# Kernel tuning notes

Measured on AMD Instinct MI355X. Metric: run time of the kernel, lower is better.

## Reference

```python
import jax, jax.numpy as jnp
import numpy as np

N_NODES = 16384
DIM = 1024
NUM_HEADS = 16
HEAD_DIM = 64
CURV = -1.0  # hyperbolic stereographic (Poincare ball) curvature, shared by all heads
EPS = 1e-15
PROJ_EPS = 4e-3  # geoopt float32 projection eps


def _clamp_abs(x, eps):
    # geoopt.utils.clamp_abs: sign-preserving clamp of |x| (sign(0) -> +1)
    s = jnp.sign(jnp.sign(x) + 0.5)
    return s * jnp.maximum(jnp.abs(x), eps)


def _artan_k(x, k):  # k < 0: artanh(sqrt(-k) x)/sqrt(-k)
    sk = jnp.sqrt(jnp.maximum(jnp.abs(k), EPS))
    return jnp.arctanh(jnp.clip(sk * x, -1.0 + 1e-7, 1.0 - 1e-7)) / sk


def _tan_k(x, k):  # k < 0: tanh(sqrt(-k) x)/sqrt(-k)
    sk = jnp.sqrt(jnp.maximum(jnp.abs(k), EPS))
    return jnp.tanh(sk * x) / sk


def _norm(x):
    return jnp.maximum(jnp.linalg.norm(x, axis=-1, keepdims=True), EPS)


def _project(x, k):
    maxnorm = (1.0 - PROJ_EPS) / jnp.sqrt(jnp.maximum(jnp.abs(k), EPS))
    n = _norm(x)
    return jnp.where(n > maxnorm, x / n * maxnorm, x)


def _mobius_scalar_mul(r, x, k):
    xn = _norm(x)
    return _tan_k(r * _artan_k(xn, k), k) * x / xn


def _mobius_matvec(W, x, k):
    xn = _norm(x)
    mx = x @ W
    mxn = _norm(mx)
    res = _tan_k(mxn / xn * _artan_k(xn, k), k) * mx / mxn
    zero = jnp.all(mx == 0, axis=-1, keepdims=True)
    return jnp.where(zero, jnp.zeros((), x.dtype), res)


def _logmap0(y, k):
    yn = _norm(y)
    return _artan_k(yn, k) * y / yn


def _expmap0(u, k):
    un = _norm(u)
    return _project(_tan_k(un, k) * u / un, k)


def _kappa_relu(x, k):
    # manifold.apply(relu): relu in tangent space at origin
    return _expmap0(jax.nn.relu(_logmap0(x, k)), k)


def _geo_lin_attn(Q, K, V, mask, k):
    # Q,K,V: (H,N,hd); mask: (N,); k: (H,1,1)
    denom_pt = jnp.maximum(1.0 + k * jnp.sum(V * V, -1, keepdims=True), EPS)  # (H,N,1)
    v1 = jax.nn.elu(Q / denom_pt) + 1.0          # parallel_transport0back(V, Q) -> elu+1
    gamma = 2.0 / denom_pt                        # lambda_x(V)
    denominator = _clamp_abs(gamma - 1.0, 1e-10)
    m = mask[None, :, None]
    x = gamma / denominator * V * m
    v2 = denominator * (jax.nn.elu(K / denom_pt) + 1.0) * m
    v2_sum = jnp.sum(v2, axis=-2)                 # (H,hd)
    D = jnp.einsum('hnd,hd->hn', v1, v2_sum)
    D_inv = 1.0 / jnp.where(D == 0, 1e-5, D)
    context = jnp.einsum('hnd,hne->hde', v2, x)   # (H,hd,hd)
    out = jnp.einsum('hde,hnd,hn->hne', context, v1, D_inv)
    out = _project(out, k)
    out = _mobius_scalar_mul(0.5, out, k)
    return _project(out, k)


def setup_inputs():
    key = jax.random.key(0)
    ks = jax.random.split(key, 6)
    kc = jnp.float32(CURV)
    X = _project(0.02 * jax.random.normal(ks[0], (N_NODES, DIM), jnp.float32), kc)
    mask = jnp.ones((N_NODES,), jnp.float32)
    hdim = NUM_HEADS * HEAD_DIM
    Wq = 0.02 * jax.random.normal(ks[1], (DIM, hdim), jnp.float32)
    bq = jnp.zeros((hdim,), jnp.float32)
    Wk = 0.02 * jax.random.normal(ks[2], (DIM, hdim), jnp.float32)
    bk = jnp.zeros((hdim,), jnp.float32)
    Wv = 0.01 * jax.random.normal(ks[3], (DIM, hdim), jnp.float32)
    Wff = 0.01 * jax.random.normal(ks[4], (hdim, DIM), jnp.float32)
    return {"X": X, "mask": mask, "Wq": Wq, "bq": bq, "Wk": Wk, "bk": bk, "Wv": Wv, "Wff": Wff}


def reference(X, mask, Wq, bq, Wk, bk, Wv, Wff):
    kc = jnp.float32(CURV)
    k_head = jnp.full((NUM_HEADS, 1, 1), CURV, X.dtype)

    def split(t):  # (N, H*hd) -> (H, N, hd)
        return t.reshape(N_NODES, NUM_HEADS, HEAD_DIM).transpose(1, 0, 2)

    Q = split(X @ Wq + bq)
    K = split(X @ Wk + bk)
    V = split(_kappa_relu(_mobius_matvec(Wv, X, kc), kc))  # KappaGCN with A_hat=None
    attn = _geo_lin_attn(Q, K, V, mask, k_head)            # (H,N,hd)
    comb = attn.transpose(1, 0, 2).reshape(N_NODES, NUM_HEADS * HEAD_DIM)
    return _kappa_relu(_mobius_matvec(Wff, comb, kc), kc)
```

## Files before the change

kernel.cpp:

```cpp
#include <hip/hip_runtime.h>
#include <hip/hip_bf16.h>
#include <math.h>

#define N_NODES 16384
#define DIMV 1024
#define NHEADS 16
#define HEADD 64

typedef __attribute__((ext_vector_type(8))) short short8;
typedef __attribute__((ext_vector_type(4))) float f32x4;
typedef unsigned short ushort_t;

#define GLD16(gptr, lptr)                                                                 \
  __builtin_amdgcn_global_load_lds((const __attribute__((address_space(1))) void*)(gptr), \
                                   (__attribute__((address_space(3))) void*)(lptr), 16, 0, 0)


__device__ __forceinline__ float waveReduceSum(float v) {
#pragma unroll
  for (int m = 32; m; m >>= 1) v += __shfl_xor(v, m);
  return v;
}

__device__ __forceinline__ float blockReduceSum(float v, float* red) {
  float w = waveReduceSum(v);
  __syncthreads();
  if ((threadIdx.x & 63) == 0) red[threadIdx.x >> 6] = w;
  __syncthreads();
  return red[0] + red[1] + red[2] + red[3];
}

__device__ __forceinline__ float elup1_fast(float z) {
  return z > 0.0f ? z + 1.0f : __expf(z);
}

__device__ __forceinline__ float clampabs(float x, float eps) {
  float s = (x >= 0.0f) ? 1.0f : -1.0f;
  return s * fmaxf(fabsf(x), eps);
}

__device__ __forceinline__ ushort_t f2b(float x) {
  unsigned u = __float_as_uint(x);
  unsigned r = (u + 0x7FFFu + ((u >> 16) & 1u)) >> 16;
  return (ushort_t)r;
}
__device__ __forceinline__ float b2f(ushort_t h) {
  return __uint_as_float(((unsigned)h) << 16);
}

__global__ __launch_bounds__(256) void cvt_norm_kernel(const float* __restrict__ src,
                                                       ushort_t* __restrict__ dst,
                                                       float* __restrict__ rowsq) {
  __shared__ float red[4];
  const int row = blockIdx.x;
  const int t = threadIdx.x;
  float4 x4 = ((const float4*)(src + (size_t)row * DIMV))[t];
  ushort_t h[4] = {f2b(x4.x), f2b(x4.y), f2b(x4.z), f2b(x4.w)};
  ((uint2*)(dst + (size_t)row * DIMV))[t] = *(uint2*)h;
  float s = x4.x * x4.x + x4.y * x4.y + x4.z * x4.z + x4.w * x4.w;
  s = blockReduceSum(s, red);
  if (t == 0) rowsq[row] = s;
}

__global__ __launch_bounds__(256) void transW_kernel(const float* __restrict__ src,
                                                     ushort_t* __restrict__ hi) {
  __shared__ float tile[32][33];
  const int bx = blockIdx.x * 32, by = blockIdx.y * 32;
  const int tx = threadIdx.x & 31, ty = threadIdx.x >> 5;
#pragma unroll
  for (int i = 0; i < 32; i += 8) tile[ty + i][tx] = src[(size_t)(by + ty + i) * DIMV + bx + tx];
  __syncthreads();
#pragma unroll
  for (int i = 0; i < 32; i += 8)
    hi[(size_t)(bx + ty + i) * DIMV + by + tx] = f2b(tile[tx][ty + i]);
}

__global__ __launch_bounds__(256) void transW3_kernel(const float* __restrict__ s0,
                                                      const float* __restrict__ s1,
                                                      const float* __restrict__ s2,
                                                      ushort_t* __restrict__ d0,
                                                      ushort_t* __restrict__ d1,
                                                      ushort_t* __restrict__ d2) {
  __shared__ float tile[32][33];
  const float* src = (blockIdx.z == 0) ? s0 : (blockIdx.z == 1) ? s1 : s2;
  ushort_t* dst = (blockIdx.z == 0) ? d0 : (blockIdx.z == 1) ? d1 : d2;
  const int bx = blockIdx.x * 32, by = blockIdx.y * 32;
  const int tx = threadIdx.x & 31, ty = threadIdx.x >> 5;
#pragma unroll
  for (int i = 0; i < 32; i += 8) tile[ty + i][tx] = src[(size_t)(by + ty + i) * DIMV + bx + tx];
  __syncthreads();
#pragma unroll
  for (int i = 0; i < 32; i += 8)
    dst[(size_t)(bx + ty + i) * DIMV + by + tx] = f2b(tile[tx][ty + i]);
}


template <int EPI, int NB>
__global__ __launch_bounds__(512, 2) void gemm_bf(const ushort_t* __restrict__ A,
                                                  const ushort_t* __restrict__ Bt,
                                                  const float* __restrict__ biasQ,
                                                  const float* __restrict__ biasK,
                                                  const float* __restrict__ denom,
                                                  const float* __restrict__ mask,
                                                  float* __restrict__ v2sum,
                                                  float* __restrict__ mxhsq,
                                                  float* __restrict__ reluhsq,
                                                  ushort_t* __restrict__ Cq,
                                                  ushort_t* __restrict__ Ck) {
  __shared__ ushort_t As[2][256 * 64];
  __shared__ ushort_t Bs[2][256 * 64];
  const int bid = blockIdx.x;
  const int nwg = NB * 64;
  const int swz = (bid & 7) * (nwg / 8) + (bid >> 3);
  const int bm = (swz / NB) * 256;
  const int bn = (swz % NB) * 256;
  const int t = threadIdx.x;
  const int w = t >> 6, lane = t & 63, l15 = lane & 15;
  const int wr = (w >> 2) * 128;
  const int wcn = (w & 3) * 64;
  const int g4 = lane >> 4;
  const int e7 = l15 & 7;
  const int uo0 = (g4 ^ e7) * 8;
  const int uo1 = ((4 + g4) ^ e7) * 8;

  const int rowin = lane >> 3;
  const int ksh = ((lane & 7) ^ ((lane >> 3) & 7)) * 8;
  const ushort_t *gA[4], *gB[4];
  int lofs[4];
#pragma unroll
  for (int c = 0; c < 4; ++c) {
    const int ch = w + 8 * c;
    lofs[c] = ch * 512;
    gA[c] = A + (size_t)(bm + ch * 8 + rowin) * DIMV + ksh;
    gB[c] = Bt + (size_t)(bn + ch * 8 + rowin) * DIMV + ksh;
  }

#define STAGE_G(buf, k0)                              \
  do {                                                \
    _Pragma("unroll") for (int c = 0; c < 4; ++c) {   \
      GLD16(gA[c] + (k0), &As[buf][lofs[c]]);         \
      GLD16(gB[c] + (k0), &Bs[buf][lofs[c]]);         \
    }                                                 \
  } while (0)

  f32x4 acc[8][4];
#pragma unroll
  for (int i = 0; i < 8; ++i)
#pragma unroll
    for (int j = 0; j < 4; ++j) acc[i][j] = (f32x4){0.f, 0.f, 0.f, 0.f};

  STAGE_G(0, 0);
  __syncthreads();
  int cur = 0;
  for (int k0 = 0; k0 < DIMV; k0 += 64) {
    if (k0 + 64 < DIMV) STAGE_G(cur ^ 1, k0 + 64);
#pragma unroll
    for (int ks = 0; ks < 2; ++ks) {
      const int uo = ks ? uo1 : uo0;
      short8 bf[4];
#pragma unroll
      for (int j = 0; j < 4; ++j)
        bf[j] = *(const short8*)&Bs[cur][(wcn + j * 16 + l15) * 64 + uo];
#pragma unroll
      for (int i = 0; i < 8; ++i) {
        short8 af = *(const short8*)&As[cur][(wr + i * 16 + l15) * 64 + uo];
#pragma unroll
        for (int j = 0; j < 4; ++j)
          acc[i][j] = __builtin_amdgcn_mfma_f32_16x16x32_bf16(af, bf[j], acc[i][j], 0, 0, 0);
      }
    }
    __syncthreads();
    cur ^= 1;
  }
#undef STAGE_G

  const int rbase = (lane >> 4) * 4;
  if (EPI == 0) {
#pragma unroll
    for (int j = 0; j < 4; ++j) {
      const int col = bn + wcn + j * 16 + l15;
#pragma unroll
      for (int i = 0; i < 8; ++i)
#pragma unroll
        for (int r = 0; r < 4; ++r)
          Cq[(size_t)(bm + wr + i * 16 + rbase + r) * DIMV + col] = f2b(acc[i][j][r]);
    }
  } else if (EPI == 4) {
    const int h = ((bn + wcn) >> 6) & (NHEADS - 1);
#pragma unroll
    for (int i = 0; i < 8; ++i) {
#pragma unroll
      for (int r = 0; r < 4; ++r) {
        const int row = bm + wr + i * 16 + rbase + r;
        float smx = 0.f, srel = 0.f;
#pragma unroll
        for (int j = 0; j < 4; ++j) {
          float val = acc[i][j][r];
          Cq[(size_t)row * DIMV + bn + wcn + j * 16 + l15] = f2b(val);
          smx = fmaf(val, val, smx);
          float rv = fmaxf(val, 0.f);
          srel = fmaf(rv, rv, srel);
        }
        smx += __shfl_xor(smx, 1); smx += __shfl_xor(smx, 2);
        smx += __shfl_xor(smx, 4); smx += __shfl_xor(smx, 8);
        srel += __shfl_xor(srel, 1); srel += __shfl_xor(srel, 2);
        srel += __shfl_xor(srel, 4); srel += __shfl_xor(srel, 8);
        if (l15 == 0) {
          mxhsq[(size_t)h * N_NODES + row] = smx;
          reluhsq[(size_t)h * N_NODES + row] = srel;
        }
      }
    }
  } else {
    const bool isK = (bn >= DIMV);
    const int h = ((bn + wcn) >> 6) & (NHEADS - 1);
    int lc[4];
    float bb[4];
#pragma unroll
    for (int j = 0; j < 4; ++j) {
      lc[j] = (bn + wcn + j * 16 + l15) & (DIMV - 1);
      bb[j] = isK ? biasK[lc[j]] : biasQ[lc[j]];
    }
    float csum[4] = {0.f, 0.f, 0.f, 0.f};
#pragma unroll
    for (int i = 0; i < 8; ++i) {
#pragma unroll
      for (int r = 0; r < 4; ++r) {
        const int row = bm + wr + i * 16 + rbase + r;
        const float invdp = 1.0f / denom[(size_t)h * N_NODES + row];
        float den = 0.f, mk = 0.f;
        if (isK) {
          den = clampabs(2.0f * invdp - 1.0f, 1e-10f);
          mk = mask[row];
        }
#pragma unroll
        for (int j = 0; j < 4; ++j) {
          float val = elup1_fast((acc[i][j][r] + bb[j]) * invdp);
          if (isK) {
            val = den * val * mk;
            csum[j] += val;
            Ck[(size_t)row * DIMV + lc[j]] = f2b(val);
          } else {
            Cq[(size_t)row * DIMV + lc[j]] = f2b(val);
          }
        }
      }
    }
    if (isK) {
#pragma unroll
      for (int j = 0; j < 4; ++j) atomicAdd(&v2sum[lc[j]], csum[j]);
    }
  }
}

__global__ __launch_bounds__(256) void vscale_kernel(const float* __restrict__ xnormsq,
                                                     const float* __restrict__ mxhsq,
                                                     const float* __restrict__ reluhsq,
                                                     float* __restrict__ scaleV,
                                                     float* __restrict__ denom) {
  const int row = blockIdx.x * 256 + threadIdx.x;
  float sm = 0.f, sr = 0.f;
  float hs[NHEADS];
#pragma unroll
  for (int h = 0; h < NHEADS; ++h) {
    sm += mxhsq[(size_t)h * N_NODES + row];
    hs[h] = reluhsq[(size_t)h * N_NODES + row];
    sr += hs[h];
  }
  float sx = xnormsq[row];
  float xn = fmaxf(sqrtf(sx), 1e-15f);
  float mxn = fmaxf(sqrtf(sm), 1e-15f);
  float cx = fminf(xn, 1.0f - 1e-7f);
  float t1 = tanhf(mxn / xn * atanhf(cx));
  float s1 = t1 / mxn;
  float yn = fmaxf(fabsf(t1), 1e-15f);
  float a = atanhf(fminf(yn, 1.0f - 1e-7f)) / yn;
  float k1 = a * s1;
  float un = fmaxf(k1 * sqrtf(sr), 1e-15f);
  float t2 = tanhf(un);
  float s2 = t2 / un;
  if (t2 > 0.996f) s2 *= 0.996f / t2;
  float sV = s2 * k1;
  scaleV[row] = sV;
#pragma unroll
  for (int h = 0; h < NHEADS; ++h)
    denom[(size_t)h * N_NODES + row] = fmaxf(1.0f - sV * sV * hs[h], 1e-15f);
}

__global__ __launch_bounds__(256) void rowtrans_kernel(const ushort_t* __restrict__ msrc,
                                                       const float* __restrict__ rowsq,
                                                       float* __restrict__ dstv) {
  __shared__ float red[4];
  const int row = blockIdx.x;
  const int t = threadIdx.x;
  uint2 mraw = ((const uint2*)(msrc + (size_t)row * DIMV))[t];
  ushort_t* mh = (ushort_t*)&mraw;
  float4 m4 = make_float4(b2f(mh[0]), b2f(mh[1]), b2f(mh[2]), b2f(mh[3]));
  float sm = m4.x * m4.x + m4.y * m4.y + m4.z * m4.z + m4.w * m4.w;
  sm = blockReduceSum(sm, red);
  float sx = rowsq[row];

  float xn = fmaxf(sqrtf(sx), 1e-15f);
  float mxn = fmaxf(sqrtf(sm), 1e-15f);
  float cx = fminf(xn, 1.0f - 1e-7f);
  float t1 = tanhf(mxn / xn * atanhf(cx));
  float s1 = t1 / mxn;

  float yn = fmaxf(fabsf(t1), 1e-15f);
  float a = atanhf(fminf(yn, 1.0f - 1e-7f)) / yn;
  float k1 = a * s1;
  float4 u = make_float4(fmaxf(k1 * m4.x, 0.0f), fmaxf(k1 * m4.y, 0.0f),
                         fmaxf(k1 * m4.z, 0.0f), fmaxf(k1 * m4.w, 0.0f));
  float su = u.x * u.x + u.y * u.y + u.z * u.z + u.w * u.w;
  su = blockReduceSum(su, red);

  float un = fmaxf(sqrtf(su), 1e-15f);
  float t2 = tanhf(un);
  float s2 = t2 / un;
  if (t2 > 0.996f) s2 *= 0.996f / t2;
  float4 o = make_float4(s2 * u.x, s2 * u.y, s2 * u.z, s2 * u.w);
  ((float4*)(dstv + (size_t)row * DIMV))[t] = o;
}

__global__ __launch_bounds__(256) void context_kernel(const ushort_t* __restrict__ v2buf,
                                                      const ushort_t* __restrict__ mxVbuf,
                                                      const float* __restrict__ scaleV,
                                                      const float* __restrict__ denom,
                                                      const float* __restrict__ mask,
                                                      float* __restrict__ ctxT) {
  __shared__ ushort_t s2T[64 * 64];
  __shared__ ushort_t sxT[64 * 64];
  const int h = blockIdx.y;
  const int t = threadIdx.x;
  const int w = t >> 6, lane = t & 63, l15 = lane & 15, g = lane >> 4;
  const int e7 = l15 & 7;
  const int uo0 = (g ^ e7) * 8;
  const int uo1 = ((4 + g) ^ e7) * 8;

  f32x4 acc[4];
#pragma unroll
  for (int j = 0; j < 4; ++j) acc[j] = (f32x4){0.f, 0.f, 0.f, 0.f};

  const int rbase = blockIdx.x * 512;
  for (int c = 0; c < 8; ++c) {
#pragma unroll
    for (int i = 0; i < 4; ++i) {
      int f = i * 256 + t;
      int r = f >> 4;
      int cc = (f & 15) * 4;
      int row = rbase + c * 64 + r;
      uint2 araw = *(const uint2*)(v2buf + (size_t)row * DIMV + h * HEADD + cc);
      ushort_t* ah = (ushort_t*)&araw;
      float dp = denom[(size_t)h * N_NODES + row];
      float gamma = 2.0f / dp;
      float den = clampabs(gamma - 1.0f, 1e-10f);
      float c1 = gamma / den * mask[row] * scaleV[row];
      uint2 braw = *(const uint2*)(mxVbuf + (size_t)row * DIMV + h * HEADD + cc);
      ushort_t* bh = (ushort_t*)&braw;
      const int rhi = r >> 3, rlo = r & 7;
#pragma unroll
      for (int q = 0; q < 4; ++q) {
        const int d = cc + q;
        const int pos = d * 64 + ((rhi ^ (d & 7)) << 3) + rlo;
        s2T[pos] = ah[q];
        sxT[pos] = f2b(c1 * fmaxf(b2f(bh[q]), 0.f));
      }
    }
    __syncthreads();
#pragma unroll
    for (int ks = 0; ks < 2; ++ks) {
      const int uo = ks ? uo1 : uo0;
      short8 af = *(const short8*)&s2T[(w * 16 + l15) * 64 + uo];
#pragma unroll
      for (int j = 0; j < 4; ++j) {
        short8 bfv = *(const short8*)&sxT[(j * 16 + l15) * 64 + uo];
        acc[j] = __builtin_amdgcn_mfma_f32_16x16x32_bf16(af, bfv, acc[j], 0, 0, 0);
      }
    }
    __syncthreads();
  }
#pragma unroll
  for (int j = 0; j < 4; ++j)
#pragma unroll
    for (int r = 0; r < 4; ++r)
      atomicAdd(&ctxT[h * 4096 + (j * 16 + l15) * 64 + w * 16 + g * 4 + r], acc[j][r]);
}

__global__ __launch_bounds__(256) void out_mfma_kernel(const ushort_t* __restrict__ v1bf,
                                                       const float* __restrict__ v2sum,
                                                       const float* __restrict__ ctxT,
                                                       ushort_t* __restrict__ combHi,
                                                       float* __restrict__ combnorm) {
  __shared__ ushort_t Blds[80][88];
  const int h = blockIdx.y;
  const int bm = blockIdx.x * 256;
  const int t = threadIdx.x;
  const int w = t >> 6, lane = t & 63, l15 = lane & 15;
  const int kk = (lane >> 4) * 8;

  for (int idx = t; idx < 80 * 64; idx += 256) {
    int e = idx >> 6, d = idx & 63;
    float v = 0.0f;
    if (e < 64) v = ctxT[h * 4096 + e * 64 + d];
    else if (e == 64) v = v2sum[h * 64 + d];
    Blds[e][d] = f2b(v);
  }
  __syncthreads();

  f32x4 acc[4][5];
#pragma unroll
  for (int i = 0; i < 4; ++i)
#pragma unroll
    for (int j = 0; j < 5; ++j) acc[i][j] = (f32x4){0.f, 0.f, 0.f, 0.f};
#pragma unroll
  for (int ks = 0; ks < 2; ++ks) {
    short8 bfr[5];
#pragma unroll
    for (int j = 0; j < 5; ++j) bfr[j] = *(const short8*)&Blds[j * 16 + l15][ks * 32 + kk];
#pragma unroll
    for (int i = 0; i < 4; ++i) {
      short8 af = *(const short8*)(v1bf + (size_t)(bm + w * 64 + i * 16 + l15) * DIMV +
                                   h * HEADD + ks * 32 + kk);
#pragma unroll
      for (int j = 0; j < 5; ++j)
        acc[i][j] = __builtin_amdgcn_mfma_f32_16x16x32_bf16(af, bfr[j], acc[i][j], 0, 0, 0);
    }
  }

  const int g4 = (lane >> 4) * 4;
#pragma unroll
  for (int i = 0; i < 4; ++i) {
#pragma unroll
    for (int r = 0; r < 4; ++r) {
      const int row = bm + w * 64 + i * 16 + g4 + r;
      float D = __shfl(acc[i][4][r], lane & 48);
      float Dinv = 1.0f / (D == 0.0f ? 1e-5f : D);
      float o[4];
      float s = 0.0f;
#pragma unroll
      for (int j = 0; j < 4; ++j) {
        o[j] = acc[i][j][r] * Dinv;
        s = fmaf(o[j], o[j], s);
      }
      s += __shfl_xor(s, 1); s += __shfl_xor(s, 2);
      s += __shfl_xor(s, 4); s += __shfl_xor(s, 8);
      float n1 = fmaxf(sqrtf(s), 1e-15f);
      float sc = 1.0f;
      if (n1 > 0.996f) sc = 0.996f / n1;
      float xn = fmaxf(fminf(n1, 0.996f), 1e-15f);
      float cx = fminf(xn, 1.0f - 1e-7f);
      float t2 = cx / (1.0f + sqrtf(1.0f - cx * cx));
      sc *= t2 / xn;
      if (l15 == 0) atomicAdd(&combnorm[row], s * sc * sc);
#pragma unroll
      for (int j = 0; j < 4; ++j) {
        float ov = o[j] * sc;
        combHi[(size_t)row * DIMV + h * HEADD + j * 16 + l15] = f2b(ov);
      }
    }
  }
}


extern "C" void kernel_launch(void* const* d_in, const int* in_sizes, int n_in,
                              void* d_out, int out_size, void* d_ws, size_t ws_size,
                              hipStream_t stream) {
  const float* X = (const float*)d_in[0];
  const float* mask = (const float*)d_in[1];
  const float* Wq = (const float*)d_in[2];
  const float* bq = (const float*)d_in[3];
  const float* Wk = (const float*)d_in[4];
  const float* bk = (const float*)d_in[5];
  const float* Wv = (const float*)d_in[6];
  const float* Wff = (const float*)d_in[7];
  float* out = (float*)d_out;

  const size_t MAT = (size_t)N_NODES * DIMV;
  char* p = (char*)d_ws;
  ushort_t* v1bf = (ushort_t*)p;
  ushort_t* mxV = (ushort_t*)(p + MAT * 2);
  float* combnorm = (float*)(p + MAT * 2);
  p += MAT * 4;
  float* xnormsq = (float*)p;
  ushort_t* v2bf = (ushort_t*)p;
  ushort_t* combHi = (ushort_t*)p;
  p += MAT * 4;
  ushort_t* WffHi = (ushort_t*)p;
  p += MAT * 2;
  ushort_t* Xbf = (ushort_t*)p;
  ushort_t* outBf = Xbf;
  p += MAT * 2;
  float* denom = (float*)p;   p += (size_t)NHEADS * N_NODES * 4;
  float* v2sum = (float*)p;   p += 1024 * 4;
  float* ctxT = (float*)p;    p += (size_t)NHEADS * 4096 * 4;
  float* mxhsq = (float*)p;   p += (size_t)NHEADS * N_NODES * 4;
  float* reluhsq = (float*)p; p += (size_t)NHEADS * N_NODES * 4;
  float* scaleV = (float*)p;  p += (size_t)N_NODES * 4;
  const size_t need = (size_t)(p - (char*)d_ws);
  if (ws_size < need) return;

  ushort_t* Wt = (ushort_t*)d_out;
  ushort_t* WtK = Wt + (size_t)DIMV * DIMV;
  ushort_t* WtV = WtK + (size_t)DIMV * DIMV;

  dim3 tgrid(32, 32);

  cvt_norm_kernel<<<N_NODES, 256, 0, stream>>>(X, Xbf, xnormsq);
  transW3_kernel<<<dim3(32, 32, 3), 256, 0, stream>>>(Wq, Wk, Wv, Wt, WtK, WtV);
  gemm_bf<4, 4><<<256, 512, 0, stream>>>(Xbf, WtV, nullptr, nullptr, nullptr, nullptr,
                                         nullptr, mxhsq, reluhsq, mxV, nullptr);
  vscale_kernel<<<N_NODES / 256, 256, 0, stream>>>(xnormsq, mxhsq, reluhsq, scaleV, denom);
  hipMemsetAsync(v2sum, 0, (1024 + 4096 * NHEADS) * sizeof(float), stream);
  gemm_bf<3, 8><<<512, 512, 0, stream>>>(Xbf, Wt, bq, bk, denom, mask, v2sum, nullptr,
                                         nullptr, v1bf, v2bf);
  context_kernel<<<dim3(32, NHEADS), 256, 0, stream>>>(v2bf, mxV, scaleV, denom, mask, ctxT);
  hipMemsetAsync(combnorm, 0, N_NODES * sizeof(float), stream);
  out_mfma_kernel<<<dim3(N_NODES / 256, NHEADS), 256, 0, stream>>>(v1bf, v2sum, ctxT, combHi,
                                                                   combnorm);
  transW_kernel<<<tgrid, 256, 0, stream>>>(Wff, WffHi);
  gemm_bf<0, 4><<<256, 512, 0, stream>>>(combHi, WffHi, nullptr, nullptr, nullptr, nullptr,
                                         nullptr, nullptr, nullptr, outBf, nullptr);
  rowtrans_kernel<<<N_NODES, 256, 0, stream>>>(outBf, combnorm, out);
}
```

Before: 350.2 us.

## Compute Q/K projection GEMM in FP8 e4m3 with swizzled layout

Converts X and the transposed Wq/Wk to scaled FP8 e4m3 in a pre-swizzled LDS-friendly layout, and runs the fused Q/K projection GEMM with fp8 MFMA instructions, descaling by 1/256 in the epilogue. It also folds the Wff transpose into the same multi-weight transpose launch, removing one kernel launch. The aim is to halve operand bytes and double MFMA throughput for the largest GEMM, at the cost of reduced precision in Q and K. The scratch layout changes (Xf8 placed in the output buffer), which risks accuracy tolerance failures.

```diff
diff --git a/kernel.cpp b/kernel.cpp
--- a/kernel.cpp
+++ b/kernel.cpp
@@ -9,7 +9,9 @@
 
 typedef __attribute__((ext_vector_type(8))) short short8;
 typedef __attribute__((ext_vector_type(4))) float f32x4;
+typedef __attribute__((ext_vector_type(2))) long long2_t;
 typedef unsigned short ushort_t;
+typedef unsigned char uchar_t;
 
 #define GLD16(gptr, lptr)                                                                 \
   __builtin_amdgcn_global_load_lds((const __attribute__((address_space(1))) void*)(gptr), \
@@ -48,8 +50,22 @@
   return __uint_as_float(((unsigned)h) << 16);
 }
 
+__device__ __forceinline__ uchar_t f2e4m3(float x) {
+  unsigned u = __float_as_uint(x);
+  unsigned s = (u >> 24) & 0x80u;
+  unsigned a = u & 0x7fffffffu;
+  if (a < 0x3c800000u) return (uchar_t)s;
+  if (a > 0x43e00000u) return (uchar_t)(s | 0x7eu);
+  unsigned lsb = (a >> 20) & 1u;
+  a += 0x7ffffu + lsb;
+  unsigned e = (a >> 23) - 120u;
+  unsigned m = (a >> 20) & 7u;
+  return (uchar_t)(s | (e << 3) | m);
+}
+
 __global__ __launch_bounds__(256) void cvt_norm_kernel(const float* __restrict__ src,
                                                        ushort_t* __restrict__ dst,
+                                                       uchar_t* __restrict__ xf8,
                                                        float* __restrict__ rowsq) {
   __shared__ float red[4];
   const int row = blockIdx.x;
@@ -57,56 +73,57 @@
   float4 x4 = ((const float4*)(src + (size_t)row * DIMV))[t];
   ushort_t h[4] = {f2b(x4.x), f2b(x4.y), f2b(x4.z), f2b(x4.w)};
   ((uint2*)(dst + (size_t)row * DIMV))[t] = *(uint2*)h;
+  unsigned pk = (unsigned)f2e4m3(x4.x * 16.f) | ((unsigned)f2e4m3(x4.y * 16.f) << 8) |
+                ((unsigned)f2e4m3(x4.z * 16.f) << 16) | ((unsigned)f2e4m3(x4.w * 16.f) << 24);
+  const int g = (t >> 1) & 3, ks = (t >> 3) & 1, k64 = t >> 4, e0 = (t & 1) << 2;
+  *(unsigned*)(xf8 + (size_t)row * DIMV + k64 * 64 + ((g ^ ((row >> 1) & 3)) << 4) +
+               (ks << 3) + e0) = pk;
   float s = x4.x * x4.x + x4.y * x4.y + x4.z * x4.z + x4.w * x4.w;
   s = blockReduceSum(s, red);
   if (t == 0) rowsq[row] = s;
 }
 
-__global__ __launch_bounds__(256) void transW_kernel(const float* __restrict__ src,
-                                                     ushort_t* __restrict__ hi) {
+__global__ __launch_bounds__(256) void transW4_kernel(const float* __restrict__ s0,
+                                                      const float* __restrict__ s1,
+                                                      const float* __restrict__ s2,
+                                                      const float* __restrict__ s3,
+                                                      uchar_t* __restrict__ d0,
+                                                      uchar_t* __restrict__ d1,
+                                                      ushort_t* __restrict__ d2,
+                                                      ushort_t* __restrict__ d3) {
   __shared__ float tile[32][33];
+  const int z = blockIdx.z;
+  const float* src = (z == 0) ? s0 : (z == 1) ? s1 : (z == 2) ? s2 : s3;
   const int bx = blockIdx.x * 32, by = blockIdx.y * 32;
   const int tx = threadIdx.x & 31, ty = threadIdx.x >> 5;
 #pragma unroll
   for (int i = 0; i < 32; i += 8) tile[ty + i][tx] = src[(size_t)(by + ty + i) * DIMV + bx + tx];
   __syncthreads();
-#pragma unroll
-  for (int i = 0; i < 32; i += 8)
-    hi[(size_t)(bx + ty + i) * DIMV + by + tx] = f2b(tile[tx][ty + i]);
-}
-
-__global__ __launch_bounds__(256) void transW3_kernel(const float* __restrict__ s0,
-                                                      const float* __restrict__ s1,
-                                                      const float* __restrict__ s2,
-                                                      ushort_t* __restrict__ d0,
-                                                      ushort_t* __restrict__ d1,
-                                                      ushort_t* __restrict__ d2) {
-  __shared__ float tile[32][33];
-  const float* src = (blockIdx.z == 0) ? s0 : (blockIdx.z == 1) ? s1 : s2;
-  ushort_t* dst = (blockIdx.z == 0) ? d0 : (blockIdx.z == 1) ? d1 : d2;
-  const int bx = blockIdx.x * 32, by = blockIdx.y * 32;
-  const int tx = threadIdx.x & 31, ty = threadIdx.x >> 5;
-#pragma unroll
-  for (int i = 0; i < 32; i += 8) tile[ty + i][tx] = src[(size_t)(by + ty + i) * DIMV + bx + tx];
-  __syncthreads();
-#pragma unroll
-  for (int i = 0; i < 32; i += 8)
-    dst[(size_t)(bx + ty + i) * DIMV + by + tx] = f2b(tile[tx][ty + i]);
+  if (z < 2) {
+    uchar_t* dst = z ? d1 : d0;
+#pragma unroll
+    for (int i = 0; i < 32; i += 8) {
+      const int n = bx + ty + i, k = by + tx;
+      const size_t byte = (size_t)n * DIMV + ((k >> 6) << 6) +
+                          ((((k >> 3) & 3) ^ ((n >> 1) & 3)) << 4) + (((k >> 5) & 1) << 3) +
+                          (k & 7);
+      dst[byte] = f2e4m3(16.f * tile[tx][ty + i]);
+    }
+  } else {
+    ushort_t* dst = (z == 2) ? d2 : d3;
+#pragma unroll
+    for (int i = 0; i < 32; i += 8)
+      dst[(size_t)(bx + ty + i) * DIMV + by + tx] = f2b(tile[tx][ty + i]);
+  }
 }
 
 
 template <int EPI, int NB>
 __global__ __launch_bounds__(512, 2) void gemm_bf(const ushort_t* __restrict__ A,
                                                   const ushort_t* __restrict__ Bt,
-                                                  const float* __restrict__ biasQ,
-                                                  const float* __restrict__ biasK,
-                                                  const float* __restrict__ denom,
-                                                  const float* __restrict__ mask,
-                                                  float* __restrict__ v2sum,
                                                   float* __restrict__ mxhsq,
                                                   float* __restrict__ reluhsq,
-                                                  ushort_t* __restrict__ Cq,
-                                                  ushort_t* __restrict__ Ck) {
+                                                  ushort_t* __restrict__ Cq) {
   __shared__ ushort_t As[2][256 * 64];
   __shared__ ushort_t Bs[2][256 * 64];
   const int bid = blockIdx.x;
@@ -185,7 +202,7 @@
         for (int r = 0; r < 4; ++r)
           Cq[(size_t)(bm + wr + i * 16 + rbase + r) * DIMV + col] = f2b(acc[i][j][r]);
     }
-  } else if (EPI == 4) {
+  } else {
     const int h = ((bn + wcn) >> 6) & (NHEADS - 1);
 #pragma unroll
     for (int i = 0; i < 8; ++i) {
@@ -211,45 +228,117 @@
         }
       }
     }
-  } else {
-    const bool isK = (bn >= DIMV);
-    const int h = ((bn + wcn) >> 6) & (NHEADS - 1);
-    int lc[4];
-    float bb[4];
-#pragma unroll
-    for (int j = 0; j < 4; ++j) {
-      lc[j] = (bn + wcn + j * 16 + l15) & (DIMV - 1);
-      bb[j] = isK ? biasK[lc[j]] : biasQ[lc[j]];
-    }
-    float csum[4] = {0.f, 0.f, 0.f, 0.f};
+  }
+}
+
+template <int NB>
+__global__ __launch_bounds__(512, 2) void gemm_f8qk(const uchar_t* __restrict__ Xf8,
+                                                    const uchar_t* __restrict__ Bt8,
+                                                    const float* __restrict__ biasQ,
+                                                    const float* __restrict__ biasK,
+                                                    const float* __restrict__ denom,
+                                                    const float* __restrict__ mask,
+                                                    float* __restrict__ v2sum,
+                                                    ushort_t* __restrict__ Cq,
+                                                    ushort_t* __restrict__ Ck) {
+  __shared__ uchar_t LB[65536];
+  const int bid = blockIdx.x;
+  const int nwg = NB * 64;
+  const int swz = (bid & 7) * (nwg / 8) + (bid >> 3);
+  const int bm = (swz / NB) * 256;
+  const int bn = (swz % NB) * 256;
+  const int t = threadIdx.x;
+  const int w = t >> 6, lane = t & 63, l15 = lane & 15;
+  const int wr = (w >> 2) * 128;
+  const int wcn = (w & 3) * 64;
+  const int g = lane >> 4;
+  const int aoff = ((g ^ ((l15 >> 1) & 3)) << 4);
+
+  const uchar_t *gA[2], *gB[2];
+  int lofs[2];
+#pragma unroll
+  for (int c = 0; c < 2; ++c) {
+    const int row = (t >> 2) + c * 128;
+    lofs[c] = t * 16 + c * 8192;
+    gA[c] = Xf8 + (size_t)(bm + row) * DIMV + (t & 3) * 16;
+    gB[c] = Bt8 + (size_t)(bn + row) * DIMV + (t & 3) * 16;
+  }
+
+#define STAGE_F(buf, kb)                                        \
+  do {                                                          \
+    _Pragma("unroll") for (int c = 0; c < 2; ++c) {             \
+      GLD16(gA[c] + (kb), &LB[(buf) * 16384 + lofs[c]]);        \
+      GLD16(gB[c] + (kb), &LB[32768 + (buf) * 16384 + lofs[c]]); \
+    }                                                           \
+  } while (0)
+
+  f32x4 acc[8][4];
+#pragma unroll
+  for (int i = 0; i < 8; ++i)
+#pragma unroll
+    for (int j = 0; j < 4; ++j) acc[i][j] = (f32x4){0.f, 0.f, 0.f, 0.f};
+
+  STAGE_F(0, 0);
+  __syncthreads();
+  int cur = 0;
+  for (int kt = 0; kt < 16; ++kt) {
+    if (kt < 15) STAGE_F(cur ^ 1, (kt + 1) * 64);
+    long2_t bf[4];
+#pragma unroll
+    for (int j = 0; j < 4; ++j)
+      bf[j] = *(const long2_t*)&LB[32768 + cur * 16384 + (wcn + j * 16 + l15) * 64 + aoff];
 #pragma unroll
     for (int i = 0; i < 8; ++i) {
-#pragma unroll
-      for (int r = 0; r < 4; ++r) {
-        const int row = bm + wr + i * 16 + rbase + r;
-        const float invdp = 1.0f / denom[(size_t)h * N_NODES + row];
-        float den = 0.f, mk = 0.f;
+      long2_t af = *(const long2_t*)&LB[cur * 16384 + (wr + i * 16 + l15) * 64 + aoff];
+#pragma unroll
+      for (int j = 0; j < 4; ++j) {
+        acc[i][j] = __builtin_amdgcn_mfma_f32_16x16x32_fp8_fp8(af.x, bf[j].x, acc[i][j], 0, 0, 0);
+        acc[i][j] = __builtin_amdgcn_mfma_f32_16x16x32_fp8_fp8(af.y, bf[j].y, acc[i][j], 0, 0, 0);
+      }
+    }
+    __syncthreads();
+    cur ^= 1;
+  }
+#undef STAGE_F
+
+  const int rbase = (lane >> 4) * 4;
+  const bool isK = (bn >= DIMV);
+  const int h = ((bn + wcn) >> 6) & (NHEADS - 1);
+  int lc[4];
+  float bb[4];
+#pragma unroll
+  for (int j = 0; j < 4; ++j) {
+    lc[j] = (bn + wcn + j * 16 + l15) & (DIMV - 1);
+    bb[j] = isK ? biasK[lc[j]] : biasQ[lc[j]];
+  }
+  float csum[4] = {0.f, 0.f, 0.f, 0.f};
+#pragma unroll
+  for (int i = 0; i < 8; ++i) {
+#pragma unroll
+    for (int r = 0; r < 4; ++r) {
+      const int row = bm + wr + i * 16 + rbase + r;
+      const float invdp = 1.0f / denom[(size_t)h * N_NODES + row];
+      float den = 0.f, mk = 0.f;
+      if (isK) {
+        den = clampabs(2.0f * invdp - 1.0f, 1e-10f);
+        mk = mask[row];
+      }
+#pragma unroll
+      for (int j = 0; j < 4; ++j) {
+        float val = elup1_fast((acc[i][j][r] * 0.00390625f + bb[j]) * invdp);
         if (isK) {
-          den = clampabs(2.0f * invdp - 1.0f, 1e-10f);
-          mk = mask[row];
+          val = den * val * mk;
+          csum[j] += val;
+          Ck[(size_t)row * DIMV + lc[j]] = f2b(val);
+        } else {
+          Cq[(size_t)row * DIMV + lc[j]] = f2b(val);
         }
-#pragma unroll
-        for (int j = 0; j < 4; ++j) {
-          float val = elup1_fast((acc[i][j][r] + bb[j]) * invdp);
-          if (isK) {
-            val = den * val * mk;
-            csum[j] += val;
-            Ck[(size_t)row * DIMV + lc[j]] = f2b(val);
-          } else {
-            Cq[(size_t)row * DIMV + lc[j]] = f2b(val);
-          }
-        }
-      }
-    }
-    if (isK) {
-#pragma unroll
-      for (int j = 0; j < 4; ++j) atomicAdd(&v2sum[lc[j]], csum[j]);
-    }
+      }
+    }
+  }
+  if (isK) {
+#pragma unroll
+    for (int j = 0; j < 4; ++j) atomicAdd(&v2sum[lc[j]], csum[j]);
   }
 }
 
@@ -483,9 +572,8 @@
   p += MAT * 4;
   float* xnormsq = (float*)p;
   ushort_t* v2bf = (ushort_t*)p;
+  p += MAT * 4;
   ushort_t* combHi = (ushort_t*)p;
-  p += MAT * 4;
-  ushort_t* WffHi = (ushort_t*)p;
   p += MAT * 2;
   ushort_t* Xbf = (ushort_t*)p;
   ushort_t* outBf = Xbf;
@@ -499,26 +587,22 @@
   const size_t need = (size_t)(p - (char*)d_ws);
   if (ws_size < need) return;
 
-  ushort_t* Wt = (ushort_t*)d_out;
-  ushort_t* WtK = Wt + (size_t)DIMV * DIMV;
-  ushort_t* WtV = WtK + (size_t)DIMV * DIMV;
-
-  dim3 tgrid(32, 32);
-
-  cvt_norm_kernel<<<N_NODES, 256, 0, stream>>>(X, Xbf, xnormsq);
-  transW3_kernel<<<dim3(32, 32, 3), 256, 0, stream>>>(Wq, Wk, Wv, Wt, WtK, WtV);
-  gemm_bf<4, 4><<<256, 512, 0, stream>>>(Xbf, WtV, nullptr, nullptr, nullptr, nullptr,
-                                         nullptr, mxhsq, reluhsq, mxV, nullptr);
+  uchar_t* Wq8 = (uchar_t*)d_out;
+  uchar_t* Wk8 = Wq8 + (size_t)DIMV * DIMV;
+  ushort_t* WtV = (ushort_t*)(Wq8 + 2 * (size_t)DIMV * DIMV);
+  ushort_t* WffT = WtV + (size_t)DIMV * DIMV;
+  uchar_t* Xf8 = (uchar_t*)d_out + 8 * 1024 * 1024;
+
+  cvt_norm_kernel<<<N_NODES, 256, 0, stream>>>(X, Xbf, Xf8, xnormsq);
+  transW4_kernel<<<dim3(32, 32, 4), 256, 0, stream>>>(Wq, Wk, Wv, Wff, Wq8, Wk8, WtV, WffT);
+  gemm_bf<4, 4><<<256, 512, 0, stream>>>(Xbf, WtV, mxhsq, reluhsq, mxV);
   vscale_kernel<<<N_NODES / 256, 256, 0, stream>>>(xnormsq, mxhsq, reluhsq, scaleV, denom);
   hipMemsetAsync(v2sum, 0, (1024 + 4096 * NHEADS) * sizeof(float), stream);
-  gemm_bf<3, 8><<<512, 512, 0, stream>>>(Xbf, Wt, bq, bk, denom, mask, v2sum, nullptr,
-                                         nullptr, v1bf, v2bf);
+  gemm_f8qk<8><<<512, 512, 0, stream>>>(Xf8, Wq8, bq, bk, denom, mask, v2sum, v1bf, v2bf);
   context_kernel<<<dim3(32, NHEADS), 256, 0, stream>>>(v2bf, mxV, scaleV, denom, mask, ctxT);
   hipMemsetAsync(combnorm, 0, N_NODES * sizeof(float), stream);
   out_mfma_kernel<<<dim3(N_NODES / 256, NHEADS), 256, 0, stream>>>(v1bf, v2sum, ctxT, combHi,
                                                                    combnorm);
-  transW_kernel<<<tgrid, 256, 0, stream>>>(Wff, WffHi);
-  gemm_bf<0, 4><<<256, 512, 0, stream>>>(combHi, WffHi, nullptr, nullptr, nullptr, nullptr,
-                                         nullptr, nullptr, nullptr, outBf, nullptr);
+  gemm_bf<0, 4><<<256, 512, 0, stream>>>(combHi, WffT, nullptr, nullptr, outBf);
   rowtrans_kernel<<<N_NODES, 256, 0, stream>>>(outBf, combnorm, out);
 }
```

New measurement: 342.0 us. -2.3%, faster.
